# Kernel tuning notes

Measured on AMD Instinct MI355X. Metric: run time of the kernel, lower is better.

The kernel has to match this reference:

```python
import jax, jax.numpy as jnp
import numpy as np

EPS = 1e-10


def setup_inputs() -> dict:
    key = jax.random.key(0)
    kx, ky = jax.random.split(key)
    x = jax.random.normal(kx, (8, 8192, 3), dtype=jnp.float32)
    y = jax.random.normal(ky, (8, 8192, 3), dtype=jnp.float32)
    return {"x": x, "y": y}


def reference(x, y):
    # x: (B, N, 3), y: (B, M, 3)
    xy = -2.0 * jnp.einsum("bnd,bmd->bnm", x, y)          # (B, N, M)
    xx = jnp.sum(x * x, axis=-1, keepdims=True)            # (B, N, 1)
    yy = jnp.sum(y * y, axis=-1, keepdims=True)            # (B, M, 1)
    dist = jnp.sqrt(xy + xx + jnp.swapaxes(yy, 1, 2) + EPS)  # (B, N, M)
    distance1 = jnp.min(dist, axis=2)                      # (B, N): x -> nearest y
    distance2 = jnp.min(dist, axis=1)                      # (B, M): y -> nearest x
    mean1 = jnp.mean(distance1, axis=-1)                   # (B,)
    mean2 = jnp.mean(distance2, axis=-1)                   # (B,)
    return jnp.sum(jnp.maximum(mean1, mean2))
```

## Files before the change

### kernel.cpp

```cpp
#include <hip/hip_runtime.h>


#define BB 8
#define NN 8192
#define BLK 256
#define CCOLS 256
#define CT 8
#define RT 4
#define STRIPS 16

typedef __attribute__((ext_vector_type(8))) short bf16x8;
typedef __attribute__((ext_vector_type(16))) float f32x16;
typedef __attribute__((ext_vector_type(4))) unsigned int u32x4;

__device__ __forceinline__ unsigned f2mono(float f) {
    unsigned u = __float_as_uint(f);
    return u ^ ((unsigned)((int)u >> 31) | 0x80000000u);
}
__device__ __forceinline__ float mono2f(unsigned m) {
    unsigned u = ((int)m >= 0) ? ~m : (m ^ 0x80000000u);
    return __uint_as_float(u);
}
__device__ __forceinline__ unsigned short bfh(float v) {
    unsigned u = __float_as_uint(v);
    u += 0x7FFFu + ((u >> 16) & 1u);
    return (unsigned short)(u >> 16);
}
__device__ __forceinline__ float bff(unsigned short h) {
    return __uint_as_float(((unsigned)h) << 16);
}
__device__ __forceinline__ unsigned pk(unsigned lo, unsigned hi) {
    return (lo & 0xFFFFu) | (hi << 16);
}

struct Limbs { unsigned h0, h1, h2, l0, l1, l2, sh, sl; };

__device__ __forceinline__ Limbs limbs(float w0, float w1, float w2, float scale) {
    float v0 = scale * w0, v1 = scale * w1, v2 = scale * w2;
    float s2 = w0*w0 + w1*w1 + w2*w2;
    Limbs L;
    L.h0 = bfh(v0); L.h1 = bfh(v1); L.h2 = bfh(v2);
    L.l0 = bfh(v0 - bff(L.h0)); L.l1 = bfh(v1 - bff(L.h1)); L.l2 = bfh(v2 - bff(L.h2));
    L.sh = bfh(s2); L.sl = bfh(s2 - bff(L.sh));
    return L;
}

__device__ __forceinline__ bf16x8 fragA(const Limbs& L, bool hi) {
    const unsigned one = 0x3F80u;
    u32x4 v;
    v[0] = hi ? pk(L.h2, L.sh) : pk(L.h0, L.h1);
    v[1] = hi ? pk(L.sl, one)  : pk(L.h2, L.l0);
    v[2] = hi ? pk(one, 0u)    : pk(L.l1, L.l2);
    v[3] = hi ? 0u             : pk(L.h0, L.h1);
    return __builtin_bit_cast(bf16x8, v);
}
__device__ __forceinline__ bf16x8 fragB(const Limbs& L, bool hi) {
    const unsigned one = 0x3F80u;
    u32x4 v;
    v[0] = hi ? pk(L.l2, one)  : pk(L.h0, L.h1);
    v[1] = hi ? pk(one, L.sh)  : pk(L.h2, L.h0);
    v[2] = hi ? pk(L.sl, 0u)   : pk(L.h1, L.h2);
    v[3] = hi ? 0u             : pk(L.l0, L.l1);
    return __builtin_bit_cast(bf16x8, v);
}

__global__ __launch_bounds__(BLK, 2) void
main_kernel(const float* __restrict__ x, const float* __restrict__ y,
            float* __restrict__ bpart) {
    __shared__ unsigned colmin[CCOLS];
    __shared__ float red[4];
    const int bi  = blockIdx.x;
    const int dir = bi >> 8;
    const int b   = (bi >> 5) & 7;
    const int cc  = bi & 31;
    const float* A  = dir ? y : x;
    const float* Bp = dir ? x : y;
    const int tid = threadIdx.x;
    const int lane = tid & 63, w = tid >> 6;
    const int m = lane & 31;
    const bool hb = (lane >> 5) != 0;

    colmin[tid] = 0xFFFFFFFFu;

    bf16x8 bf[CT];
#pragma unroll
    for (int ct = 0; ct < CT; ++ct) {
        int c = b * NN + cc * CCOLS + ct * 32 + m;
        bf[ct] = fragB(limbs(Bp[3*c], Bp[3*c+1], Bp[3*c+2], 1.f), hb);
    }

    f32x16 zro;
#pragma unroll
    for (int i = 0; i < 16; ++i) zro[i] = 0.f;

    float rm[CT];
#pragma unroll
    for (int ct = 0; ct < CT; ++ct) rm[ct] = 3.4e38f;

#pragma unroll 1
    for (int s = 0; s < STRIPS; ++s) {
        bf16x8 af[RT];
#pragma unroll
        for (int t = 0; t < RT; ++t) {
            int r = b * NN + s * 512 + w * 128 + t * 32 + m;
            af[t] = fragA(limbs(A[3*r], A[3*r+1], A[3*r+2], -2.f), hb);
        }
#pragma unroll
        for (int ct = 0; ct < CT; ++ct) {
            f32x16 a0 = __builtin_amdgcn_mfma_f32_32x32x16_bf16(af[0], bf[ct], zro, 0, 0, 0);
            f32x16 a1 = __builtin_amdgcn_mfma_f32_32x32x16_bf16(af[1], bf[ct], zro, 0, 0, 0);
            f32x16 a2 = __builtin_amdgcn_mfma_f32_32x32x16_bf16(af[2], bf[ct], zro, 0, 0, 0);
            f32x16 a3 = __builtin_amdgcn_mfma_f32_32x32x16_bf16(af[3], bf[ct], zro, 0, 0, 0);
            float p = rm[ct];
#pragma unroll
            for (int r = 0; r < 16; ++r) {
                float t0 = fminf(fminf(a0[r], a1[r]), a2[r]);
                p = fminf(fminf(t0, a3[r]), p);
            }
            rm[ct] = p;
        }
    }

#pragma unroll
    for (int ct = 0; ct < CT; ++ct) {
        float p = fminf(rm[ct], __shfl_xor(rm[ct], 32, 64));
        if (!hb) atomicMin(&colmin[ct * 32 + m], f2mono(p));
    }
    __syncthreads();

    float d = sqrtf(fmaxf(mono2f(colmin[tid]), 0.f) + 1e-10f);
#pragma unroll
    for (int off = 32; off; off >>= 1) d += __shfl_down(d, off, 64);
    if (lane == 0) red[w] = d;
    __syncthreads();
    if (tid == 0) bpart[bi] = red[0] + red[1] + red[2] + red[3];
}

__global__ void fin_kernel(const float* __restrict__ bpart, float* __restrict__ out) {
    __shared__ float g[16];
    const int t = threadIdx.x;
    float v = bpart[t];
#pragma unroll
    for (int off = 16; off; off >>= 1) v += __shfl_down(v, off, 32);
    if ((t & 31) == 0) g[t >> 5] = v;
    __syncthreads();
    if (t == 0) {
        float acc = 0.f;
        for (int b = 0; b < BB; ++b) acc += fmaxf(g[b], g[BB + b]);
        out[0] = acc * (1.0f / (float)NN);
    }
}

extern "C" void kernel_launch(void* const* d_in, const int* in_sizes, int n_in,
                              void* d_out, int out_size, void* d_ws, size_t ws_size,
                              hipStream_t stream) {
    const float* x = (const float*)d_in[0];
    const float* y = (const float*)d_in[1];
    float* out = (float*)d_out;
    float* bpart = (float*)d_ws;

    main_kernel<<<512, BLK, 0, stream>>>(x, y, bpart);
    fin_kernel<<<1, 512, 0, stream>>>(bpart, out);
}
```

Baseline: 104.1 us.

## Precompute bf16 MFMA fragments in prep kernel, prefetch rows, fuse final reduction

Adds a prep kernel that converts every point of x and y once into split-bf16 A and B fragments and stores them in workspace, so the main kernel no longer rebuilds limbs for each strip. The main loop double-buffers the A fragments, loading the next strip while the MFMAs for the current one run. The separate finalize kernel is dropped: the last block to finish, found with an atomic counter, does the cross-block reduction. This swaps redundant ALU work for extra global traffic plus one prep launch, and relies on fence and atomic ordering for the last-block reduction to be correct.

```diff
diff --git a/kernel.cpp b/kernel.cpp
--- a/kernel.cpp
+++ b/kernel.cpp
@@ -3,6 +3,7 @@
 
 #define BB 8
 #define NN 8192
+#define NPTS (BB*NN)
 #define BLK 256
 #define CCOLS 256
 #define CT 8
@@ -11,7 +12,6 @@
 
 typedef __attribute__((ext_vector_type(8))) short bf16x8;
 typedef __attribute__((ext_vector_type(16))) float f32x16;
-typedef __attribute__((ext_vector_type(4))) unsigned int u32x4;
 
 __device__ __forceinline__ unsigned f2mono(float f) {
     unsigned u = __float_as_uint(f);
@@ -21,64 +21,60 @@
     unsigned u = ((int)m >= 0) ? ~m : (m ^ 0x80000000u);
     return __uint_as_float(u);
 }
-__device__ __forceinline__ unsigned short bfh(float v) {
+__device__ __forceinline__ unsigned bfh(float v) {
     unsigned u = __float_as_uint(v);
     u += 0x7FFFu + ((u >> 16) & 1u);
-    return (unsigned short)(u >> 16);
+    return u >> 16;
 }
-__device__ __forceinline__ float bff(unsigned short h) {
-    return __uint_as_float(((unsigned)h) << 16);
+__device__ __forceinline__ float bff(unsigned h) {
+    return __uint_as_float(h << 16);
 }
 __device__ __forceinline__ unsigned pk(unsigned lo, unsigned hi) {
     return (lo & 0xFFFFu) | (hi << 16);
 }
 
-struct Limbs { unsigned h0, h1, h2, l0, l1, l2, sh, sl; };
-
-__device__ __forceinline__ Limbs limbs(float w0, float w1, float w2, float scale) {
-    float v0 = scale * w0, v1 = scale * w1, v2 = scale * w2;
-    float s2 = w0*w0 + w1*w1 + w2*w2;
-    Limbs L;
-    L.h0 = bfh(v0); L.h1 = bfh(v1); L.h2 = bfh(v2);
-    L.l0 = bfh(v0 - bff(L.h0)); L.l1 = bfh(v1 - bff(L.h1)); L.l2 = bfh(v2 - bff(L.h2));
-    L.sh = bfh(s2); L.sl = bfh(s2 - bff(L.sh));
-    return L;
+__global__ void prep_kernel(const float* __restrict__ x, const float* __restrict__ y,
+                            uint4* __restrict__ afr, uint4* __restrict__ bfr,
+                            unsigned* __restrict__ counter) {
+    int i = blockIdx.x * BLK + threadIdx.x;
+    if (i == 0) *counter = 0;
+    const float* src = (i < NPTS) ? x : y;
+    int j = (i < NPTS) ? i : i - NPTS;
+    float c0 = src[3*j], c1 = src[3*j+1], c2 = src[3*j+2];
+    float s2 = c0*c0 + c1*c1 + c2*c2;
+    unsigned sh = bfh(s2), sl = bfh(s2 - bff(sh));
+    float a0 = -2.f*c0, a1 = -2.f*c1, a2 = -2.f*c2;
+    unsigned ah0 = bfh(a0), ah1 = bfh(a1), ah2 = bfh(a2);
+    unsigned al0 = bfh(a0 - bff(ah0)), al1 = bfh(a1 - bff(ah1)), al2 = bfh(a2 - bff(ah2));
+    unsigned bh0 = bfh(c0), bh1 = bfh(c1), bh2 = bfh(c2);
+    unsigned bl0 = bfh(c0 - bff(bh0)), bl1 = bfh(c1 - bff(bh1)), bl2 = bfh(c2 - bff(bh2));
+    const unsigned one = 0x3F80u;
+    afr[2*i]   = make_uint4(pk(ah0,ah1), pk(ah2,al0), pk(al1,al2), pk(ah0,ah1));
+    afr[2*i+1] = make_uint4(pk(ah2,sh),  pk(sl,one),  pk(one,0u),  0u);
+    bfr[2*i]   = make_uint4(pk(bh0,bh1), pk(bh2,bh0), pk(bh1,bh2), pk(bl0,bl1));
+    bfr[2*i+1] = make_uint4(pk(bl2,one), pk(one,sh),  pk(sl,0u),   0u);
 }
 
-__device__ __forceinline__ bf16x8 fragA(const Limbs& L, bool hi) {
-    const unsigned one = 0x3F80u;
-    u32x4 v;
-    v[0] = hi ? pk(L.h2, L.sh) : pk(L.h0, L.h1);
-    v[1] = hi ? pk(L.sl, one)  : pk(L.h2, L.l0);
-    v[2] = hi ? pk(one, 0u)    : pk(L.l1, L.l2);
-    v[3] = hi ? 0u             : pk(L.h0, L.h1);
-    return __builtin_bit_cast(bf16x8, v);
-}
-__device__ __forceinline__ bf16x8 fragB(const Limbs& L, bool hi) {
-    const unsigned one = 0x3F80u;
-    u32x4 v;
-    v[0] = hi ? pk(L.l2, one)  : pk(L.h0, L.h1);
-    v[1] = hi ? pk(one, L.sh)  : pk(L.h2, L.h0);
-    v[2] = hi ? pk(L.sl, 0u)   : pk(L.h1, L.h2);
-    v[3] = hi ? 0u             : pk(L.l0, L.l1);
-    return __builtin_bit_cast(bf16x8, v);
-}
+__device__ __forceinline__ bf16x8 cvt(uint4 v) { return __builtin_bit_cast(bf16x8, v); }
 
 __global__ __launch_bounds__(BLK, 2) void
-main_kernel(const float* __restrict__ x, const float* __restrict__ y,
-            float* __restrict__ bpart) {
+main_kernel(const uint4* __restrict__ afr, const uint4* __restrict__ bfr,
+            float* __restrict__ bpart, unsigned* __restrict__ counter,
+            float* __restrict__ out) {
     __shared__ unsigned colmin[CCOLS];
     __shared__ float red[4];
+    __shared__ float gg[8];
+    __shared__ int lastflag;
     const int bi  = blockIdx.x;
     const int dir = bi >> 8;
     const int b   = (bi >> 5) & 7;
     const int cc  = bi & 31;
-    const float* A  = dir ? y : x;
-    const float* Bp = dir ? x : y;
+    const uint4* Af = afr + (dir ? 2*NPTS : 0);
+    const uint4* Bf = bfr + (dir ? 0 : 2*NPTS);
     const int tid = threadIdx.x;
     const int lane = tid & 63, w = tid >> 6;
     const int m = lane & 31;
-    const bool hb = (lane >> 5) != 0;
+    const int hb = lane >> 5;
 
     colmin[tid] = 0xFFFFFFFFu;
 
@@ -86,7 +82,7 @@
 #pragma unroll
     for (int ct = 0; ct < CT; ++ct) {
         int c = b * NN + cc * CCOLS + ct * 32 + m;
-        bf[ct] = fragB(limbs(Bp[3*c], Bp[3*c+1], Bp[3*c+2], 1.f), hb);
+        bf[ct] = cvt(Bf[2*c + hb]);
     }
 
     f32x16 zro;
@@ -97,20 +93,22 @@
 #pragma unroll
     for (int ct = 0; ct < CT; ++ct) rm[ct] = 3.4e38f;
 
+    const int rowbase = b * NN + w * 128 + m;
+    uint4 cur[RT], nxt[RT];
+#pragma unroll
+    for (int t = 0; t < RT; ++t) cur[t] = Af[2*(rowbase + t*32) + hb];
+
 #pragma unroll 1
     for (int s = 0; s < STRIPS; ++s) {
-        bf16x8 af[RT];
+        const int np = (s + 1 < STRIPS) ? (s + 1) : s;
 #pragma unroll
-        for (int t = 0; t < RT; ++t) {
-            int r = b * NN + s * 512 + w * 128 + t * 32 + m;
-            af[t] = fragA(limbs(A[3*r], A[3*r+1], A[3*r+2], -2.f), hb);
-        }
+        for (int t = 0; t < RT; ++t) nxt[t] = Af[2*(rowbase + np*512 + t*32) + hb];
 #pragma unroll
         for (int ct = 0; ct < CT; ++ct) {
-            f32x16 a0 = __builtin_amdgcn_mfma_f32_32x32x16_bf16(af[0], bf[ct], zro, 0, 0, 0);
-            f32x16 a1 = __builtin_amdgcn_mfma_f32_32x32x16_bf16(af[1], bf[ct], zro, 0, 0, 0);
-            f32x16 a2 = __builtin_amdgcn_mfma_f32_32x32x16_bf16(af[2], bf[ct], zro, 0, 0, 0);
-            f32x16 a3 = __builtin_amdgcn_mfma_f32_32x32x16_bf16(af[3], bf[ct], zro, 0, 0, 0);
+            f32x16 a0 = __builtin_amdgcn_mfma_f32_32x32x16_bf16(cvt(cur[0]), bf[ct], zro, 0, 0, 0);
+            f32x16 a1 = __builtin_amdgcn_mfma_f32_32x32x16_bf16(cvt(cur[1]), bf[ct], zro, 0, 0, 0);
+            f32x16 a2 = __builtin_amdgcn_mfma_f32_32x32x16_bf16(cvt(cur[2]), bf[ct], zro, 0, 0, 0);
+            f32x16 a3 = __builtin_amdgcn_mfma_f32_32x32x16_bf16(cvt(cur[3]), bf[ct], zro, 0, 0, 0);
             float p = rm[ct];
 #pragma unroll
             for (int r = 0; r < 16; ++r) {
@@ -119,12 +117,14 @@
             }
             rm[ct] = p;
         }
+#pragma unroll
+        for (int t = 0; t < RT; ++t) cur[t] = nxt[t];
     }
 
 #pragma unroll
     for (int ct = 0; ct < CT; ++ct) {
         float p = fminf(rm[ct], __shfl_xor(rm[ct], 32, 64));
-        if (!hb) atomicMin(&colmin[ct * 32 + m], f2mono(p));
+        if (hb == 0) atomicMin(&colmin[ct * 32 + m], f2mono(p));
     }
     __syncthreads();
 
@@ -133,21 +133,31 @@
     for (int off = 32; off; off >>= 1) d += __shfl_down(d, off, 64);
     if (lane == 0) red[w] = d;
     __syncthreads();
-    if (tid == 0) bpart[bi] = red[0] + red[1] + red[2] + red[3];
-}
+    if (tid == 0) {
+        float total = red[0] + red[1] + red[2] + red[3];
+        atomicExch(&bpart[bi], total);
+        __threadfence();
+        unsigned old = atomicAdd(counter, 1u);
+        lastflag = (old == 511u);
+    }
+    __syncthreads();
 
-__global__ void fin_kernel(const float* __restrict__ bpart, float* __restrict__ out) {
-    __shared__ float g[16];
-    const int t = threadIdx.x;
-    float v = bpart[t];
+    if (lastflag) {
+        float v0 = atomicAdd(&bpart[tid], 0.f);
+        float v1 = atomicAdd(&bpart[256 + tid], 0.f);
 #pragma unroll
-    for (int off = 16; off; off >>= 1) v += __shfl_down(v, off, 32);
-    if ((t & 31) == 0) g[t >> 5] = v;
-    __syncthreads();
-    if (t == 0) {
-        float acc = 0.f;
-        for (int b = 0; b < BB; ++b) acc += fmaxf(g[b], g[BB + b]);
-        out[0] = acc * (1.0f / (float)NN);
+        for (int off = 16; off; off >>= 1) {
+            v0 += __shfl_down(v0, off, 32);
+            v1 += __shfl_down(v1, off, 32);
+        }
+        if ((tid & 31) == 0) gg[tid >> 5] = fmaxf(v0, v1);
+        __syncthreads();
+        if (tid == 0) {
+            float acc = 0.f;
+#pragma unroll
+            for (int k = 0; k < 8; ++k) acc += gg[k];
+            out[0] = acc * (1.0f / (float)NN);
+        }
     }
 }
 
@@ -157,8 +167,13 @@
     const float* x = (const float*)d_in[0];
     const float* y = (const float*)d_in[1];
     float* out = (float*)d_out;
-    float* bpart = (float*)d_ws;
 
-    main_kernel<<<512, BLK, 0, stream>>>(x, y, bpart);
-    fin_kernel<<<1, 512, 0, stream>>>(bpart, out);
+    char* ws = (char*)d_ws;
+    uint4* afr = (uint4*)ws;
+    uint4* bfr = afr + 4 * NPTS;
+    float* bpart = (float*)(bfr + 4 * NPTS);
+    unsigned* counter = (unsigned*)(bpart + 512);
+
+    prep_kernel<<<(2 * NPTS) / BLK, BLK, 0, stream>>>(x, y, afr, bfr, counter);
+    main_kernel<<<512, BLK, 0, stream>>>(afr, bfr, bpart, counter, out);
 }
```

After: 102.0 us. 1.02x faster.
